# Optimization experiments

Hardware: AMD Instinct MI355X
Metric: run time of the kernel (lower is better)

## Reference

```python
import jax, jax.numpy as jnp
import numpy as np

D_MODEL = 1024
N_HEADS = 16
HEAD_DIM = D_MODEL // N_HEADS


def setup_inputs() -> dict:
    key = jax.random.key(0)
    k1, k2, k3 = jax.random.split(key, 3)
    B, T, C = 4, 2048, D_MODEL
    x = jax.random.normal(k1, (B, T, C), dtype=jnp.float32)
    # torch Linear weight is (out,in); store as (in,out) so y = x @ W
    w_qkv = jax.random.normal(k2, (C, 3 * C), dtype=jnp.float32) * (1.0 / np.sqrt(C))
    w_proj = jax.random.normal(k3, (C, C), dtype=jnp.float32) * (1.0 / np.sqrt(C))
    return {"x": x, "w_qkv": w_qkv, "w_proj": w_proj}


def reference(x, w_qkv, w_proj):
    B, T, C = x.shape
    H, Dh = N_HEADS, HEAD_DIM
    qkv = x @ w_qkv                        # (B,T,3C)
    q, k, v = jnp.split(qkv, 3, axis=-1)
    def heads(t):
        return t.reshape(B, T, H, Dh).transpose(0, 2, 1, 3)  # (B,H,T,Dh)
    q, k, v = heads(q), heads(k), heads(v)
    scores = jnp.einsum('bhqd,bhkd->bhqk', q, k) / np.sqrt(Dh).astype(np.float32)
    causal = jnp.tril(jnp.ones((T, T), dtype=bool))
    scores = jnp.where(causal, scores, -jnp.inf)
    attn = jax.nn.softmax(scores, axis=-1)
    y = jnp.einsum('bhqk,bhkd->bhqd', attn, v)  # (B,H,T,Dh)
    y = y.transpose(0, 2, 1, 3).reshape(B, T, C)
    return y @ w_proj
```

## Files before the change

kernel.cpp:

```cpp
#include <hip/hip_runtime.h>

#define SEQ_T 2048
#define NBATCH 4
#define CDIM 1024
#define NHEAD 16
#define MROWS 8192
#define QKVC 3072

typedef unsigned short u16;
typedef __bf16 bf16x8 __attribute__((ext_vector_type(8)));
typedef float f32x4 __attribute__((ext_vector_type(4)));
typedef unsigned short u16x8 __attribute__((ext_vector_type(8)));
typedef unsigned uint32x4 __attribute__((ext_vector_type(4)));

__device__ __forceinline__ u16 f32_to_bf16(float f) {
  union { float f; unsigned int u; } v; v.f = f;
  unsigned int u = v.u;
  unsigned int r = ((u >> 16) & 1u) + 0x7fffu;
  return (u16)((u + r) >> 16);
}

__device__ __forceinline__ void gload_lds16(const u16* g, u16* l) {
  __builtin_amdgcn_global_load_lds(
      (const __attribute__((address_space(1))) void*)g,
      (__attribute__((address_space(3))) void*)l, 16, 0, 0);
}

__global__ __launch_bounds__(256) void cast_bf16_kernel(const float* __restrict__ in,
                                                        u16* __restrict__ out, int n4) {
  int i = blockIdx.x * 256 + threadIdx.x;
  if (i >= n4) return;
  float4 v = ((const float4*)in)[i];
  ushort4 o;
  o.x = f32_to_bf16(v.x); o.y = f32_to_bf16(v.y);
  o.z = f32_to_bf16(v.z); o.w = f32_to_bf16(v.w);
  ((ushort4*)out)[i] = o;
}

__global__ void transpose_cast_kernel(const float* __restrict__ in, u16* __restrict__ out,
                                      int R, int Cc) {
  __shared__ float tile[32][33];
  int c0 = blockIdx.x * 32, r0 = blockIdx.y * 32;
  int tx = threadIdx.x, ty = threadIdx.y;
  #pragma unroll
  for (int i = 0; i < 32; i += 8)
    tile[ty + i][tx] = in[(size_t)(r0 + ty + i) * Cc + c0 + tx];
  __syncthreads();
  #pragma unroll
  for (int i = 0; i < 32; i += 8)
    out[(size_t)(c0 + ty + i) * R + r0 + tx] = f32_to_bf16(tile[tx][ty + i]);
}

__global__ __launch_bounds__(256) void repack_k_kernel(const u16* __restrict__ QKV,
                                                       u16* __restrict__ Kc) {
  const int kvt32 = blockIdx.x, bh = blockIdx.y;
  const int b = bh >> 4, h = bh & 15;
  const int tid = threadIdx.x;
  const int f = tid >> 6, l = tid & 63;
  const int t = f >> 1, i = f & 1;
  const int row = kvt32 * 32 + t * 16 + (l & 15);
  const bf16x8 v = *(const bf16x8*)(QKV + (size_t)b * SEQ_T * QKVC + (size_t)row * QKVC +
                                    CDIM + h * 64 + i * 32 + (l >> 4) * 8);
  *(bf16x8*)(Kc + (size_t)bh * 131072 + (size_t)kvt32 * 2048 + f * 512 + l * 8) = v;
}

__global__ void repack_v_kernel(const u16* __restrict__ QKV, u16* __restrict__ Vc) {
  __shared__ u16 tile[32][34];
  const int t0 = blockIdx.x * 32, d0 = blockIdx.y * 32;
  const int bh = blockIdx.z;
  const int b = bh >> 4, h = bh & 15;
  const int tx = threadIdx.x, ty = threadIdx.y;
  const u16* Vp = QKV + (size_t)b * SEQ_T * QKVC + 2 * CDIM + h * 64 + d0;
  #pragma unroll
  for (int i = 0; i < 32; i += 8)
    tile[ty + i][tx] = Vp[(size_t)(t0 + ty + i) * QKVC + tx];
  __syncthreads();
  const int tid = ty * 32 + tx;
  if (tid < 128) {
    const int bc = tid >> 2, ag = tid & 3;
    union { u16 u[8]; bf16x8 v; } o;
    #pragma unroll
    for (int j = 0; j < 8; ++j) o.u[j] = tile[ag * 8 + j][bc];
    const int dvl = d0 + bc;
    *(bf16x8*)(Vc + (size_t)bh * 131072 + (size_t)(t0 >> 5) * 2048 +
               (dvl >> 4) * 512 + ag * 128 + (dvl & 15) * 8) = o.v;
  }
}

template <typename OT, bool QSCALE>
__global__ __launch_bounds__(256, 3)
void gemm_bt_kernel(const u16* __restrict__ A, const u16* __restrict__ Bt,
                    OT* __restrict__ C, int N, int K) {
  __shared__ u16 sA[3][4096];
  __shared__ u16 sB[3][4096];
  const int tid = threadIdx.x;
  const int lane = tid & 63, w = tid >> 6;
  const int wm = w >> 1, wn = w & 1;
  const int l15 = lane & 15, lhi = lane >> 4;
  const int row0 = blockIdx.x * 128, col0 = blockIdx.y * 128;

  const int oln  = ((lane & 3) - (lane >> 2)) & 3;
  const int srow = w * 32 + (lane >> 2);
  const u16* aS = A  + (size_t)(row0 + srow) * K + oln * 8;
  const u16* bS = Bt + (size_t)(col0 + srow) * K + oln * 8;
  const int stD = w * 1024;
  const int rdA = (wm * 64 + l15) * 32 + ((lhi + l15) & 3) * 8;
  const int rdB = (wn * 64 + l15) * 32 + ((lhi + l15) & 3) * 8;

  f32x4 acc[4][4] = {};

#define STAGE(KT, S)                                                            \
  {                                                                             \
    const size_t ko = (size_t)(KT) * 32;                                        \
    gload_lds16(aS + ko,          &sA[S][stD]);                                 \
    gload_lds16(aS + ko + 16 * K, &sA[S][stD + 512]);                           \
    gload_lds16(bS + ko,          &sB[S][stD]);                                 \
    gload_lds16(bS + ko + 16 * K, &sB[S][stD + 512]);                           \
  }
#define COMPUTE(S)                                                              \
  {                                                                             \
    bf16x8 af[4], bf[4];                                                        \
    _Pragma("unroll") for (int mi = 0; mi < 4; ++mi)                            \
      af[mi] = *(const bf16x8*)&sA[S][rdA + mi * 512];                          \
    _Pragma("unroll") for (int ni = 0; ni < 4; ++ni)                            \
      bf[ni] = *(const bf16x8*)&sB[S][rdB + ni * 512];                          \
    __builtin_amdgcn_s_setprio(1);                                              \
    _Pragma("unroll") for (int mi = 0; mi < 4; ++mi)                            \
      _Pragma("unroll") for (int ni = 0; ni < 4; ++ni)                          \
        acc[mi][ni] = __builtin_amdgcn_mfma_f32_16x16x32_bf16(af[mi], bf[ni],   \
                                                              acc[mi][ni], 0, 0, 0); \
    __builtin_amdgcn_s_setprio(0);                                              \
  }
#define WAITBAR4                                                                \
  asm volatile("s_waitcnt vmcnt(4)" ::: "memory");                              \
  __builtin_amdgcn_sched_barrier(0);                                            \
  __builtin_amdgcn_s_barrier();

  STAGE(0, 0);
  STAGE(1, 1);
  WAITBAR4;

  #pragma unroll 1
  for (int kt = 0; kt < 30; kt += 3) {
    STAGE(kt + 2, 2); COMPUTE(0); WAITBAR4;
    STAGE(kt + 3, 0); COMPUTE(1); WAITBAR4;
    STAGE(kt + 4, 1); COMPUTE(2); WAITBAR4;
  }
  COMPUTE(0);
  asm volatile("s_waitcnt vmcnt(0)" ::: "memory");
  __builtin_amdgcn_sched_barrier(0);
  __builtin_amdgcn_s_barrier();
  COMPUTE(1);
#undef STAGE
#undef COMPUTE
#undef WAITBAR4

  #pragma unroll
  for (int mt = 0; mt < 4; ++mt)
    #pragma unroll
    for (int nt = 0; nt < 4; ++nt)
      #pragma unroll
      for (int r = 0; r < 4; ++r) {
        const int rr = row0 + wm * 64 + mt * 16 + lhi * 4 + r;
        const int cc = col0 + wn * 64 + nt * 16 + l15;
        float v = acc[mt][nt][r];
        if (QSCALE && cc < CDIM) v *= 0.18033688011f;
        if constexpr (sizeof(OT) == 2) C[(size_t)rr * N + cc] = f32_to_bf16(v);
        else                           C[(size_t)rr * N + cc] = v;
      }
}

template <bool DOMASK>
__device__ __forceinline__ void attn_step(const bf16x8 (&qf)[2],
                                          const bf16x8 (&kf)[2][2],
                                          const bf16x8 (&vb)[4],
                                          const bf16x8 ones,
                                          f32x4 (&acc)[4], f32x4& acc1,
                                          int l15, int lhi, int kv0, int qg) {
  f32x4 st[2];
  #pragma unroll
  for (int t = 0; t < 2; ++t) {
    f32x4 z = {0.f, 0.f, 0.f, 0.f};
    z = __builtin_amdgcn_mfma_f32_16x16x32_bf16(kf[t][0], qf[0], z, 0, 0, 0);
    z = __builtin_amdgcn_mfma_f32_16x16x32_bf16(kf[t][1], qf[1], z, 0, 0, 0);
    st[t] = z;
  }
  #pragma unroll
  for (int t = 0; t < 2; ++t)
    #pragma unroll
    for (int r = 0; r < 4; ++r) {
      float sv = st[t][r];
      if (DOMASK) {
        const int kvg = kv0 + t * 16 + lhi * 4 + r;
        sv = (kvg > qg) ? -__builtin_inff() : sv;
      }
      st[t][r] = exp2f(sv);
    }
  unsigned c00, c01, c10, c11;
  asm("v_cvt_pk_bf16_f32 %0, %1, %2" : "=v"(c00) : "v"(st[0][0]), "v"(st[0][1]));
  asm("v_cvt_pk_bf16_f32 %0, %1, %2" : "=v"(c01) : "v"(st[0][2]), "v"(st[0][3]));
  asm("v_cvt_pk_bf16_f32 %0, %1, %2" : "=v"(c10) : "v"(st[1][0]), "v"(st[1][1]));
  asm("v_cvt_pk_bf16_f32 %0, %1, %2" : "=v"(c11) : "v"(st[1][2]), "v"(st[1][3]));
  asm("v_permlane32_swap_b32 %0, %1" : "+v"(c00), "+v"(c10));
  asm("v_permlane32_swap_b32 %0, %1" : "+v"(c01), "+v"(c11));
  asm("v_permlane16_swap_b32 %0, %1" : "+v"(c00), "+v"(c10));
  asm("v_permlane16_swap_b32 %0, %1" : "+v"(c01), "+v"(c11));
  uint32x4 pw; pw[0] = c00; pw[1] = c01; pw[2] = c10; pw[3] = c11;
  const bf16x8 pa = __builtin_bit_cast(bf16x8, pw);
  #pragma unroll
  for (int d = 0; d < 4; ++d)
    acc[d] = __builtin_amdgcn_mfma_f32_16x16x32_bf16(pa, vb[d], acc[d], 0, 0, 0);
  acc1 = __builtin_amdgcn_mfma_f32_16x16x32_bf16(pa, ones, acc1, 0, 0, 0);
}

__global__ __launch_bounds__(256, 4) void attn_kernel(const u16* __restrict__ QKV,
                                                      const u16* __restrict__ Kc,
                                                      const u16* __restrict__ Vc,
                                                      u16* __restrict__ Y) {
  __shared__ u16 Kl[2][2048];
  __shared__ u16 Vl[2][2048];
  const int tid = threadIdx.x, lane = tid & 63, wid = tid >> 6;
  const int l15 = lane & 15, lhi = lane >> 4;
  const int id = blockIdx.x;
  const int xcd = id & 7, k = (id >> 3) & 15, hi3 = id >> 7;
  const int bh = hi3 * 8 + xcd;
  const int b = bh >> 4, h = bh & 15;
  const int pa = k * 4 + wid;
  const int qA0 = pa * 16, qB0 = (127 - pa) * 16;
  const int nchA = pa / 2 + 1, nchB = (127 - pa) / 2 + 1;
  const int ncmax = (127 - k * 4) / 2 + 1;
  const size_t base = (size_t)b * SEQ_T * QKVC;
  const u16* Qp  = QKV + base + h * 64;
  const u16* KcC = Kc + (size_t)bh * 131072;
  const u16* VcC = Vc + (size_t)bh * 131072;

  u16x8 ou;
  #pragma unroll
  for (int j = 0; j < 8; ++j) ou[j] = 0x3F80;
  const bf16x8 ones = __builtin_bit_cast(bf16x8, ou);

  gload_lds16(KcC + wid * 512 + lane * 8, &Kl[0][wid * 512]);
  gload_lds16(VcC + wid * 512 + lane * 8, &Vl[0][wid * 512]);

  bf16x8 qfA[2], qfB[2];
  #pragma unroll
  for (int i = 0; i < 2; ++i) {
    qfA[i] = *(const bf16x8*)(Qp + (size_t)(qA0 + l15) * QKVC + i * 32 + lhi * 8);
    qfB[i] = *(const bf16x8*)(Qp + (size_t)(qB0 + l15) * QKVC + i * 32 + lhi * 8);
  }
  const int qgA = qA0 + l15, qgB = qB0 + l15;

  f32x4 accA[4] = {}, accB[4] = {};
  f32x4 acc1A = {}, acc1B = {};

  asm volatile("s_waitcnt vmcnt(0)" ::: "memory");
  __builtin_amdgcn_sched_barrier(0);
  __builtin_amdgcn_s_barrier();

  int cbuf = 0;
  #pragma unroll 1
  for (int ic = 0; ic < ncmax; ++ic) {
    if (ic + 1 < ncmax) {
      const u16* kg = KcC + (size_t)(ic + 1) * 2048 + wid * 512 + lane * 8;
      const u16* vg = VcC + (size_t)(ic + 1) * 2048 + wid * 512 + lane * 8;
      gload_lds16(kg, &Kl[cbuf ^ 1][wid * 512]);
      gload_lds16(vg, &Vl[cbuf ^ 1][wid * 512]);
      asm volatile("s_waitcnt vmcnt(2)" ::: "memory");
    } else {
      asm volatile("s_waitcnt vmcnt(0)" ::: "memory");
    }
    __builtin_amdgcn_sched_barrier(0);
    __builtin_amdgcn_s_barrier();

    const u16* kb = &Kl[cbuf][0];
    const u16* vp = &Vl[cbuf][0];
    bf16x8 kf[2][2], vb[4];
    #pragma unroll
    for (int t = 0; t < 2; ++t)
      #pragma unroll
      for (int i = 0; i < 2; ++i)
        kf[t][i] = *(const bf16x8*)(kb + (t * 2 + i) * 512 + lane * 8);
    #pragma unroll
    for (int d = 0; d < 4; ++d)
      vb[d] = *(const bf16x8*)(vp + d * 512 + lane * 8);

    const int kv0 = ic * 32;
    if (ic < nchB) {
      if (ic == nchB - 1)
        attn_step<true>(qfB, kf, vb, ones, accB, acc1B, l15, lhi, kv0, qgB);
      else
        attn_step<false>(qfB, kf, vb, ones, accB, acc1B, l15, lhi, kv0, qgB);
    }
    if (ic < nchA) {
      if (ic == nchA - 1)
        attn_step<true>(qfA, kf, vb, ones, accA, acc1A, l15, lhi, kv0, qgA);
      else
        attn_step<false>(qfA, kf, vb, ones, accA, acc1A, l15, lhi, kv0, qgA);
    }
    __builtin_amdgcn_s_barrier();
    cbuf ^= 1;
  }

  u16* Yp = Y + (size_t)b * SEQ_T * CDIM + h * 64;
  #pragma unroll
  for (int r = 0; r < 4; ++r) {
    const float ivA = 1.0f / acc1A[r];
    const float ivB = 1.0f / acc1B[r];
    #pragma unroll
    for (int d = 0; d < 4; ++d) {
      Yp[(size_t)(qA0 + lhi * 4 + r) * CDIM + d * 16 + l15] = f32_to_bf16(accA[d][r] * ivA);
      Yp[(size_t)(qB0 + lhi * 4 + r) * CDIM + d * 16 + l15] = f32_to_bf16(accB[d][r] * ivB);
    }
  }
}

extern "C" void kernel_launch(void* const* d_in, const int* in_sizes, int n_in,
                              void* d_out, int out_size, void* d_ws, size_t ws_size,
                              hipStream_t stream) {
  const float* x      = (const float*)d_in[0];
  const float* w_qkv  = (const float*)d_in[1];
  const float* w_proj = (const float*)d_in[2];
  float* out = (float*)d_out;

  u16* Xb  = (u16*)d_ws;
  u16* Wqt = Xb  + (size_t)MROWS * CDIM;
  u16* Wpt = Wqt + (size_t)QKVC * CDIM;
  u16* QKV = Wpt + (size_t)CDIM * CDIM;
  u16* Yb  = QKV + (size_t)MROWS * QKVC;
  u16* Vc  = Yb  + (size_t)MROWS * CDIM;
  u16* Kc  = Xb;

  cast_bf16_kernel<<<(MROWS * CDIM / 4 + 255) / 256, 256, 0, stream>>>(x, Xb, MROWS * CDIM / 4);
  transpose_cast_kernel<<<dim3(QKVC / 32, CDIM / 32), dim3(32, 8), 0, stream>>>(w_qkv, Wqt, CDIM, QKVC);
  transpose_cast_kernel<<<dim3(CDIM / 32, CDIM / 32), dim3(32, 8), 0, stream>>>(w_proj, Wpt, CDIM, CDIM);

  gemm_bt_kernel<u16, true><<<dim3(MROWS / 128, QKVC / 128), 256, 0, stream>>>(Xb, Wqt, QKV, QKVC, CDIM);

  repack_k_kernel<<<dim3(SEQ_T / 32, NBATCH * NHEAD), 256, 0, stream>>>(QKV, Kc);
  repack_v_kernel<<<dim3(SEQ_T / 32, 2, NBATCH * NHEAD), dim3(32, 8), 0, stream>>>(QKV, Vc);

  attn_kernel<<<1024, 256, 0, stream>>>(QKV, Kc, Vc, Yb);

  gemm_bt_kernel<float, false><<<dim3(MROWS / 128, CDIM / 128), 256, 0, stream>>>(Yb, Wpt, out, CDIM, CDIM);
}
```

Before: 190.0 us.

## Give each attention wave one query tile and double the grid

Each wave now owns a single 16-row query tile instead of a paired front/back pair. Four waves per block are assigned tiles 2g, 2g+1, 127-2g and 126-2g, so the block's total causal work stays balanced. The grid doubles to 2048 blocks and launch bounds rise to 6 blocks per CU. Fewer live accumulators per wave should allow higher occupancy and better latency hiding. The cost is that K/V chunks are staged through LDS by twice as many blocks, and waves whose range finishes early sit idle at the barriers until the block's longest tile is done.

```diff
diff --git a/kernel.cpp b/kernel.cpp
--- a/kernel.cpp
+++ b/kernel.cpp
@@ -213,7 +213,7 @@
   acc1 = __builtin_amdgcn_mfma_f32_16x16x32_bf16(pa, ones, acc1, 0, 0, 0);
 }
 
-__global__ __launch_bounds__(256, 4) void attn_kernel(const u16* __restrict__ QKV,
+__global__ __launch_bounds__(256, 6) void attn_kernel(const u16* __restrict__ QKV,
                                                       const u16* __restrict__ Kc,
                                                       const u16* __restrict__ Vc,
                                                       u16* __restrict__ Y) {
@@ -222,13 +222,14 @@
   const int tid = threadIdx.x, lane = tid & 63, wid = tid >> 6;
   const int l15 = lane & 15, lhi = lane >> 4;
   const int id = blockIdx.x;
-  const int xcd = id & 7, k = (id >> 3) & 15, hi3 = id >> 7;
+  const int xcd = id & 7, g = (id >> 3) & 31, hi3 = id >> 8;
   const int bh = hi3 * 8 + xcd;
   const int b = bh >> 4, h = bh & 15;
-  const int pa = k * 4 + wid;
-  const int qA0 = pa * 16, qB0 = (127 - pa) * 16;
-  const int nchA = pa / 2 + 1, nchB = (127 - pa) / 2 + 1;
-  const int ncmax = (127 - k * 4) / 2 + 1;
+  const int jw = (wid == 0) ? 2 * g : (wid == 1) ? 2 * g + 1
+               : (wid == 2) ? 127 - 2 * g : 126 - 2 * g;
+  const int q0 = jw * 16;
+  const int nch = jw / 2 + 1;
+  const int ncmax = 64 - g;
   const size_t base = (size_t)b * SEQ_T * QKVC;
   const u16* Qp  = QKV + base + h * 64;
   const u16* KcC = Kc + (size_t)bh * 131072;
@@ -242,16 +243,14 @@
   gload_lds16(KcC + wid * 512 + lane * 8, &Kl[0][wid * 512]);
   gload_lds16(VcC + wid * 512 + lane * 8, &Vl[0][wid * 512]);
 
-  bf16x8 qfA[2], qfB[2];
-  #pragma unroll
-  for (int i = 0; i < 2; ++i) {
-    qfA[i] = *(const bf16x8*)(Qp + (size_t)(qA0 + l15) * QKVC + i * 32 + lhi * 8);
-    qfB[i] = *(const bf16x8*)(Qp + (size_t)(qB0 + l15) * QKVC + i * 32 + lhi * 8);
-  }
-  const int qgA = qA0 + l15, qgB = qB0 + l15;
-
-  f32x4 accA[4] = {}, accB[4] = {};
-  f32x4 acc1A = {}, acc1B = {};
+  bf16x8 qf[2];
+  #pragma unroll
+  for (int i = 0; i < 2; ++i)
+    qf[i] = *(const bf16x8*)(Qp + (size_t)(q0 + l15) * QKVC + i * 32 + lhi * 8);
+  const int qg = q0 + l15;
+
+  f32x4 acc[4] = {};
+  f32x4 acc1 = {};
 
   asm volatile("s_waitcnt vmcnt(0)" ::: "memory");
   __builtin_amdgcn_sched_barrier(0);
@@ -272,30 +271,24 @@
     __builtin_amdgcn_sched_barrier(0);
     __builtin_amdgcn_s_barrier();
 
-    const u16* kb = &Kl[cbuf][0];
-    const u16* vp = &Vl[cbuf][0];
-    bf16x8 kf[2][2], vb[4];
-    #pragma unroll
-    for (int t = 0; t < 2; ++t)
+    if (ic < nch) {
+      const u16* kb = &Kl[cbuf][0];
+      const u16* vp = &Vl[cbuf][0];
+      bf16x8 kf[2][2], vb[4];
       #pragma unroll
-      for (int i = 0; i < 2; ++i)
-        kf[t][i] = *(const bf16x8*)(kb + (t * 2 + i) * 512 + lane * 8);
-    #pragma unroll
-    for (int d = 0; d < 4; ++d)
-      vb[d] = *(const bf16x8*)(vp + d * 512 + lane * 8);
-
-    const int kv0 = ic * 32;
-    if (ic < nchB) {
-      if (ic == nchB - 1)
-        attn_step<true>(qfB, kf, vb, ones, accB, acc1B, l15, lhi, kv0, qgB);
+      for (int t = 0; t < 2; ++t)
+        #pragma unroll
+        for (int i = 0; i < 2; ++i)
+          kf[t][i] = *(const bf16x8*)(kb + (t * 2 + i) * 512 + lane * 8);
+      #pragma unroll
+      for (int d = 0; d < 4; ++d)
+        vb[d] = *(const bf16x8*)(vp + d * 512 + lane * 8);
+
+      const int kv0 = ic * 32;
+      if (ic == nch - 1)
+        attn_step<true>(qf, kf, vb, ones, acc, acc1, l15, lhi, kv0, qg);
       else
-        attn_step<false>(qfB, kf, vb, ones, accB, acc1B, l15, lhi, kv0, qgB);
-    }
-    if (ic < nchA) {
-      if (ic == nchA - 1)
-        attn_step<true>(qfA, kf, vb, ones, accA, acc1A, l15, lhi, kv0, qgA);
-      else
-        attn_step<false>(qfA, kf, vb, ones, accA, acc1A, l15, lhi, kv0, qgA);
+        attn_step<false>(qf, kf, vb, ones, acc, acc1, l15, lhi, kv0, qg);
     }
     __builtin_amdgcn_s_barrier();
     cbuf ^= 1;
@@ -304,13 +297,10 @@
   u16* Yp = Y + (size_t)b * SEQ_T * CDIM + h * 64;
   #pragma unroll
   for (int r = 0; r < 4; ++r) {
-    const float ivA = 1.0f / acc1A[r];
-    const float ivB = 1.0f / acc1B[r];
+    const float iv = 1.0f / acc1[r];
     #pragma unroll
-    for (int d = 0; d < 4; ++d) {
-      Yp[(size_t)(qA0 + lhi * 4 + r) * CDIM + d * 16 + l15] = f32_to_bf16(accA[d][r] * ivA);
-      Yp[(size_t)(qB0 + lhi * 4 + r) * CDIM + d * 16 + l15] = f32_to_bf16(accB[d][r] * ivB);
-    }
+    for (int d = 0; d < 4; ++d)
+      Yp[(size_t)(q0 + lhi * 4 + r) * CDIM + d * 16 + l15] = f32_to_bf16(acc[d][r] * iv);
   }
 }
 
@@ -339,7 +329,7 @@
   repack_k_kernel<<<dim3(SEQ_T / 32, NBATCH * NHEAD), 256, 0, stream>>>(QKV, Kc);
   repack_v_kernel<<<dim3(SEQ_T / 32, 2, NBATCH * NHEAD), dim3(32, 8), 0, stream>>>(QKV, Vc);
 
-  attn_kernel<<<1024, 256, 0, stream>>>(QKV, Kc, Vc, Yb);
+  attn_kernel<<<2048, 256, 0, stream>>>(QKV, Kc, Vc, Yb);
 
   gemm_bt_kernel<float, false><<<dim3(MROWS / 128, CDIM / 128), 256, 0, stream>>>(Yb, Wpt, out, CDIM, CDIM);
 }
```

Result: slower. 204.4 us (+7.6%).
